# Kernel optimization log

Measured on AMD Instinct MI355X. Metric: run time of the kernel, lower is better.

The kernel has to match this reference:

```python
import jax, jax.numpy as jnp
import numpy as np

B, T = 16, 8192                       # batch, padded tokens per image
NUM_BINS, IN_CH = 4, 3
TOKEN_DIM = NUM_BINS ** 2 * (IN_CH + 2)   # 'interpolate', drop_delta=False -> 80
EMB_DIM = 384


def setup_inputs() -> dict:
    key = jax.random.key(0)
    k1, k2, k3, k4 = jax.random.split(key, 4)
    feat = jax.random.normal(k1, (B * T, TOKEN_DIM), dtype=jnp.float32)
    amask = jax.random.randint(k2, (B, T), 0, 2).astype(bool)
    amask = amask.at[:, 0].set(True)               # cls slot always valid
    g_idx = (jnp.arange(B, dtype=jnp.int32) * T)   # row index of cls token per image
    b_idx = jnp.repeat(jnp.arange(B, dtype=jnp.int32), T)
    W = jax.random.normal(k3, (EMB_DIM, TOKEN_DIM), dtype=jnp.float32) / np.sqrt(TOKEN_DIM).astype(np.float32)
    bias = jax.random.normal(k4, (EMB_DIM,), dtype=jnp.float32) * 0.001  # bias.data.mul_(0.001)
    cls_token = jnp.full((EMB_DIM,), 1e-5, dtype=jnp.float32)            # zeros + 1e-5
    return dict(feat=feat, amask=amask, g_idx=g_idx, b_idx=b_idx,
                W=W, bias=bias, cls_token=cls_token)


def reference(feat, amask, g_idx, b_idx, W, bias, cls_token):
    # MaskedLinear: gather masked rows -> linear -> scatter into zeros.
    # Equivalent dense form: compute y everywhere, zero out unmasked rows
    # (identity activation, so f(x)@W = masked-gather result exactly).
    mask = amask.reshape(-1)                                 # [B*T]
    y = feat @ W.T + bias                                    # [B*T, EMB_DIM]
    out = jnp.where(mask[:, None], y, jnp.zeros((), y.dtype))
    # cls-token insert: feat[g_idx] = cls_token (expanded over batch)
    out = out.at[g_idx].set(jnp.broadcast_to(cls_token, (g_idx.shape[0], EMB_DIM)))
    return out, amask, g_idx, b_idx
```

## Files before the change

### kernel.cpp

```cpp
#include <hip/hip_runtime.h>

#define TK 80
#define TN 384
#define BM 64

typedef __attribute__((ext_vector_type(8)))  __bf16 bf16x8;
typedef __attribute__((ext_vector_type(16))) float  f32x16;

__device__ __forceinline__ bf16x8 pack8(float4 f0, float4 f1) {
    bf16x8 r;
    r[0] = (__bf16)f0.x; r[1] = (__bf16)f0.y;
    r[2] = (__bf16)f0.z; r[3] = (__bf16)f0.w;
    r[4] = (__bf16)f1.x; r[5] = (__bf16)f1.y;
    r[6] = (__bf16)f1.z; r[7] = (__bf16)f1.w;
    return r;
}

__global__ __launch_bounds__(256) void tok_fused(
    const float* __restrict__ feat,
    const unsigned char* __restrict__ amask,
    const int* __restrict__ gidx,
    const int* __restrict__ bidx,
    const float* __restrict__ W,
    const float* __restrict__ bias,
    const float* __restrict__ cls,
    float* __restrict__ out,
    float* __restrict__ out_amask,
    float* __restrict__ out_gidx,
    float* __restrict__ out_bidx,
    int B, int T)
{
    const int tid   = threadIdx.x;
    const int lane  = tid & 63;
    const int wave  = tid >> 6;
    const int row0  = blockIdx.x * BM;
    const int colb  = wave * 96;
    const int lrow  = lane & 31;
    const int khalf = lane >> 5;

    const unsigned int* w32 = (const unsigned int*)amask;
    unsigned int wprobe = w32[tid & 255];
    int bytemode = __syncthreads_or((int)((wprobe & 0xFFFFFF00u) != 0u));

    if (tid < BM) {
        int r = row0 + tid;
        out_amask[r] = bytemode ? (float)amask[r] : (float)(w32[r] & 1u);
        out_bidx[r]  = (float)bidx[r];
    }
    if (blockIdx.x == 0 && tid < B) out_gidx[tid] = (float)gidx[tid];

    float mv;
    {
        int r = row0 + lane;
        mv = bytemode ? (float)amask[r] : (float)(w32[r] & 1u);
    }

    float bv[3], cv[3];
    #pragma unroll
    for (int nt = 0; nt < 3; ++nt) {
        int c = colb + nt * 32 + lrow;
        bv[nt] = bias[c];
        cv[nt] = cls[c];
    }

    f32x16 acc[2][3];
    #pragma unroll
    for (int mt = 0; mt < 2; ++mt)
        #pragma unroll
        for (int nt = 0; nt < 3; ++nt)
            acc[mt][nt] = (f32x16)0.0f;

    #pragma unroll
    for (int ks = 0; ks < 5; ++ks) {
        const int koff = ks * 16 + khalf * 8;

        bf16x8 af[2];
        #pragma unroll
        for (int mt = 0; mt < 2; ++mt) {
            const float* p = feat + (size_t)(row0 + mt * 32 + lrow) * TK + koff;
            af[mt] = pack8(*(const float4*)p, *(const float4*)(p + 4));
        }

        bf16x8 wf[3];
        #pragma unroll
        for (int nt = 0; nt < 3; ++nt) {
            const float* p = W + (size_t)(colb + nt * 32 + lrow) * TK + koff;
            wf[nt] = pack8(*(const float4*)p, *(const float4*)(p + 4));
        }

        #pragma unroll
        for (int mt = 0; mt < 2; ++mt)
            #pragma unroll
            for (int nt = 0; nt < 3; ++nt)
                acc[mt][nt] = __builtin_amdgcn_mfma_f32_32x32x16_bf16(
                    af[mt], wf[nt], acc[mt][nt], 0, 0, 0);
    }

    #pragma unroll
    for (int mt = 0; mt < 2; ++mt) {
        #pragma unroll
        for (int reg = 0; reg < 16; ++reg) {
            const int rlocal = mt * 32 + 4 * khalf + (reg & 3) + 8 * (reg >> 2);
            const float m = __shfl(mv, rlocal);
            const int row = row0 + rlocal;
            const bool iscls = (row % T) == 0;
            float* orow = out + (size_t)row * TN;
            #pragma unroll
            for (int nt = 0; nt < 3; ++nt) {
                float v = m * (acc[mt][nt][reg] + bv[nt]);
                if (iscls) v = cv[nt];
                orow[colb + nt * 32 + lrow] = v;
            }
        }
    }
}

extern "C" void kernel_launch(void* const* d_in, const int* in_sizes, int n_in,
                              void* d_out, int out_size, void* d_ws, size_t ws_size,
                              hipStream_t stream) {
    const float*         feat  = (const float*)d_in[0];
    const unsigned char* amask = (const unsigned char*)d_in[1];
    const int*           gidx  = (const int*)d_in[2];
    const int*           bidx  = (const int*)d_in[3];
    const float*         W     = (const float*)d_in[4];
    const float*         bias  = (const float*)d_in[5];
    const float*         cls   = (const float*)d_in[6];

    const int BT = in_sizes[1];
    const int B  = in_sizes[2];
    const int T  = BT / B;

    float* out       = (float*)d_out;
    float* out_amask = out + (size_t)BT * TN;
    float* out_gidx  = out_amask + BT;
    float* out_bidx  = out_gidx + B;

    tok_fused<<<BT / BM, 256, 0, stream>>>(
        feat, amask, gidx, bidx, W, bias, cls,
        out, out_amask, out_gidx, out_bidx, B, T);
}
```

Measured before the change: 60.76 us.

## Stage feat tile in LDS as bf16 and loop over N tiles per wave

The feat tile for the block is loaded once with coalesced float4 reads, converted to bf16 and stored in shared memory in MFMA fragment order. Each of the four waves previously re-read the same feat rows from global memory, and those duplicate loads are now replaced by LDS reads. The N dimension is processed one 32-column tile at a time, so only two accumulators are live instead of six, and launch_bounds asks for 4 blocks per CU to raise occupancy. The cls check is also simplified to a per-block test, which adds an LDS barrier and interleaves stores with compute per N tile.

```diff
diff --git a/kernel.cpp b/kernel.cpp
--- a/kernel.cpp
+++ b/kernel.cpp
@@ -5,6 +5,7 @@
 #define BM 64
 
 typedef __attribute__((ext_vector_type(8)))  __bf16 bf16x8;
+typedef __attribute__((ext_vector_type(4)))  __bf16 bf16x4;
 typedef __attribute__((ext_vector_type(16))) float  f32x16;
 
 __device__ __forceinline__ bf16x8 pack8(float4 f0, float4 f1) {
@@ -16,7 +17,7 @@
     return r;
 }
 
-__global__ __launch_bounds__(256) void tok_fused(
+__global__ __launch_bounds__(256, 4) void tok_fused(
     const float* __restrict__ feat,
     const unsigned char* __restrict__ amask,
     const int* __restrict__ gidx,
@@ -30,6 +31,8 @@
     float* __restrict__ out_bidx,
     int B, int T)
 {
+    __shared__ __align__(16) __bf16 sA[2 * 5 * 2 * 32 * 8];
+
     const int tid   = threadIdx.x;
     const int lane  = tid & 63;
     const int wave  = tid >> 6;
@@ -55,61 +58,62 @@
         mv = bytemode ? (float)amask[r] : (float)(w32[r] & 1u);
     }
 
-    float bv[3], cv[3];
     #pragma unroll
-    for (int nt = 0; nt < 3; ++nt) {
-        int c = colb + nt * 32 + lrow;
-        bv[nt] = bias[c];
-        cv[nt] = cls[c];
+    for (int i = 0; i < 5; ++i) {
+        int idx = tid + i * 256;
+        float4 v = *(const float4*)(feat + (size_t)row0 * TK + (size_t)idx * 4);
+        int rg = idx / 20;
+        int q  = idx % 20;
+        int ks = q >> 2, kh = (q >> 1) & 1, jq = q & 1;
+        int off = (((((rg >> 5) * 5 + ks) * 2 + kh) * 32 + (rg & 31)) * 8) + jq * 4;
+        bf16x4 c;
+        c[0] = (__bf16)v.x; c[1] = (__bf16)v.y;
+        c[2] = (__bf16)v.z; c[3] = (__bf16)v.w;
+        *(bf16x4*)&sA[off] = c;
     }
+    __syncthreads();
 
-    f32x16 acc[2][3];
+    bf16x8 af[2][5];
     #pragma unroll
     for (int mt = 0; mt < 2; ++mt)
         #pragma unroll
-        for (int nt = 0; nt < 3; ++nt)
-            acc[mt][nt] = (f32x16)0.0f;
+        for (int ks = 0; ks < 5; ++ks)
+            af[mt][ks] = *(const bf16x8*)
+                &sA[((((mt * 5 + ks) * 2 + khalf) * 32) + lrow) * 8];
+
+    const bool blkcls = (row0 % T) == 0;
 
     #pragma unroll
-    for (int ks = 0; ks < 5; ++ks) {
-        const int koff = ks * 16 + khalf * 8;
+    for (int nt = 0; nt < 3; ++nt) {
+        const int c = colb + nt * 32 + lrow;
 
-        bf16x8 af[2];
+        bf16x8 wf[5];
+        #pragma unroll
+        for (int ks = 0; ks < 5; ++ks) {
+            const float* p = W + (size_t)c * TK + ks * 16 + khalf * 8;
+            wf[ks] = pack8(*(const float4*)p, *(const float4*)(p + 4));
+        }
+
+        f32x16 acc0 = (f32x16)0.0f, acc1 = (f32x16)0.0f;
+        #pragma unroll
+        for (int ks = 0; ks < 5; ++ks) {
+            acc0 = __builtin_amdgcn_mfma_f32_32x32x16_bf16(af[0][ks], wf[ks], acc0, 0, 0, 0);
+            acc1 = __builtin_amdgcn_mfma_f32_32x32x16_bf16(af[1][ks], wf[ks], acc1, 0, 0, 0);
+        }
+
+        const float bvn = bias[c];
+        const float cvn = cls[c];
+
         #pragma unroll
         for (int mt = 0; mt < 2; ++mt) {
-            const float* p = feat + (size_t)(row0 + mt * 32 + lrow) * TK + koff;
-            af[mt] = pack8(*(const float4*)p, *(const float4*)(p + 4));
-        }
-
-        bf16x8 wf[3];
-        #pragma unroll
-        for (int nt = 0; nt < 3; ++nt) {
-            const float* p = W + (size_t)(colb + nt * 32 + lrow) * TK + koff;
-            wf[nt] = pack8(*(const float4*)p, *(const float4*)(p + 4));
-        }
-
-        #pragma unroll
-        for (int mt = 0; mt < 2; ++mt)
+            const f32x16& a = mt ? acc1 : acc0;
             #pragma unroll
-            for (int nt = 0; nt < 3; ++nt)
-                acc[mt][nt] = __builtin_amdgcn_mfma_f32_32x32x16_bf16(
-                    af[mt], wf[nt], acc[mt][nt], 0, 0, 0);
-    }
-
-    #pragma unroll
-    for (int mt = 0; mt < 2; ++mt) {
-        #pragma unroll
-        for (int reg = 0; reg < 16; ++reg) {
-            const int rlocal = mt * 32 + 4 * khalf + (reg & 3) + 8 * (reg >> 2);
-            const float m = __shfl(mv, rlocal);
-            const int row = row0 + rlocal;
-            const bool iscls = (row % T) == 0;
-            float* orow = out + (size_t)row * TN;
-            #pragma unroll
-            for (int nt = 0; nt < 3; ++nt) {
-                float v = m * (acc[mt][nt][reg] + bv[nt]);
-                if (iscls) v = cv[nt];
-                orow[colb + nt * 32 + lrow] = v;
+            for (int reg = 0; reg < 16; ++reg) {
+                const int rlocal = mt * 32 + 4 * khalf + (reg & 3) + 8 * (reg >> 2);
+                const float m = __shfl(mv, rlocal);
+                float v = m * (a[reg] + bvn);
+                if (blkcls & (rlocal == 0)) v = cvn;
+                out[(size_t)(row0 + rlocal) * TN + c] = v;
             }
         }
     }
```

Measured after the change: 120.6 us. 98.5% more time.
